# Performance work log

Measured on AMD Instinct MI355X. Metric: run time of the kernel, lower is better.

Reference implementation:

```python
import jax, jax.numpy as jnp
import numpy as np

H = 16  # heads


def setup_inputs() -> dict:
    key = jax.random.key(0)
    ks = jax.random.split(key, 10)
    B, S, M = 4, 2048, 1024
    scale = 1.0 / np.sqrt(M)
    return {
        "x": jax.random.normal(ks[0], (B, S, M), dtype=jnp.float32),
        "mask": jax.random.uniform(ks[1], (B, 1, S, S), dtype=jnp.float32),
        "Wq": jax.random.normal(ks[2], (M, M), dtype=jnp.float32) * scale,
        "bq": jax.random.normal(ks[3], (M,), dtype=jnp.float32) * scale,
        "Wk": jax.random.normal(ks[4], (M, M), dtype=jnp.float32) * scale,
        "bk": jax.random.normal(ks[5], (M,), dtype=jnp.float32) * scale,
        "Wv": jax.random.normal(ks[6], (M, M), dtype=jnp.float32) * scale,
        "bv": jax.random.normal(ks[7], (M,), dtype=jnp.float32) * scale,
        "Wo": jax.random.normal(ks[8], (M, M), dtype=jnp.float32) * scale,
        "bo": jax.random.normal(ks[9], (M,), dtype=jnp.float32) * scale,
    }


def reference(x, mask, Wq, bq, Wk, bk, Wv, bv, Wo, bo):
    B, S, M = x.shape
    dk = M // H
    # QKV projections (torch Linear: x @ W.T + b), then split heads -> [B,H,S,dk]
    q = (x @ Wq.T + bq).reshape(B, S, H, dk).transpose(0, 2, 1, 3)
    k = (x @ Wk.T + bk).reshape(B, S, H, dk).transpose(0, 2, 1, 3)
    v = (x @ Wv.T + bv).reshape(B, S, H, dk).transpose(0, 2, 1, 3)
    # scores: [B,H,S,S], multiplicative mask (non-standard!) then softmax
    scores = jnp.einsum("bhqd,bhkd->bhqk", q, k) / jnp.sqrt(jnp.float32(dk))
    scores = scores * mask  # mask broadcasts over heads
    attn = jax.nn.softmax(scores, axis=-1)
    # dropout is identity in eval/reference mode
    out = jnp.einsum("bhqk,bhkd->bhqd", attn, v)  # [B,H,S,dk]
    concat = out.transpose(0, 2, 1, 3).reshape(B, S, M)
    return concat @ Wo.T + bo
```

## Files before the change

kernel.cpp:

```cpp
#include <hip/hip_runtime.h>

typedef __attribute__((ext_vector_type(8))) short s16x8;
typedef __attribute__((ext_vector_type(4))) float f32x4;
typedef __attribute__((ext_vector_type(16))) float f32x16;
typedef __attribute__((ext_vector_type(2))) unsigned int u32x2;

#define DEV static __device__ __forceinline__

DEV void gload_lds16(const void* g, void* l) {
  __builtin_amdgcn_global_load_lds(
      (const __attribute__((address_space(1))) void*)g,
      (__attribute__((address_space(3))) void*)l, 16, 0, 0);
}

DEV unsigned short f2bf(float f) {
  unsigned int u = __float_as_uint(f);
  u = (u + 0x7fffu + ((u >> 16) & 1u)) >> 16;
  return (unsigned short)u;
}

DEV unsigned pk2(float lo, float hi) {
  unsigned r;
  asm("v_cvt_pk_bf16_f32 %0, %1, %2" : "=v"(r) : "v"(lo), "v"(hi));
  return r;
}

DEV float exp2_fast(float x) {
  float r;
  asm("v_exp_f32 %0, %1" : "=v"(r) : "v"(x));
  return r;
}

DEV void cvt8(const float* __restrict__ in, unsigned short* __restrict__ out, int i) {
  float4 a = *(const float4*)(in + i);
  float4 b = *(const float4*)(in + i + 4);
  union { s16x8 v; unsigned short u[8]; } o;
  o.u[0] = f2bf(a.x); o.u[1] = f2bf(a.y); o.u[2] = f2bf(a.z); o.u[3] = f2bf(a.w);
  o.u[4] = f2bf(b.x); o.u[5] = f2bf(b.y); o.u[6] = f2bf(b.z); o.u[7] = f2bf(b.w);
  *(s16x8*)(out + i) = o.v;
}

__global__ __launch_bounds__(256) void k_cvt(const float* __restrict__ in,
                                             unsigned short* __restrict__ out) {
  cvt8(in, out, (blockIdx.x * 256 + threadIdx.x) * 8);
}

__global__ __launch_bounds__(256) void k_cvt4(
    const float* __restrict__ a0, const float* __restrict__ a1,
    const float* __restrict__ a2, const float* __restrict__ a3,
    unsigned short* __restrict__ o0, unsigned short* __restrict__ o1,
    unsigned short* __restrict__ o2, unsigned short* __restrict__ o3) {
  const float* in; unsigned short* out;
  switch (blockIdx.y) {
    case 0: in = a0; out = o0; break;
    case 1: in = a1; out = o1; break;
    case 2: in = a2; out = o2; break;
    default: in = a3; out = o3; break;
  }
  cvt8(in, out, (blockIdx.x * 256 + threadIdx.x) * 8);
}

template <int MODE>
__global__ __launch_bounds__(256) void k_gemm(
    const unsigned short* __restrict__ A,
    const unsigned short* __restrict__ B0, const unsigned short* __restrict__ B1,
    const unsigned short* __restrict__ B2,
    const float* __restrict__ bias0, const float* __restrict__ bias1,
    const float* __restrict__ bias2,
    void* __restrict__ out0, void* __restrict__ out1, void* __restrict__ out2) {
  constexpr int K = 1024;
  __shared__ unsigned short As[128 * 64];
  __shared__ unsigned short Bs[128 * 64];

  const int z = blockIdx.z;
  const unsigned short* Bw = (z == 0) ? B0 : (z == 1) ? B1 : B2;
  const float* bias = (z == 0) ? bias0 : (z == 1) ? bias1 : bias2;
  void* outp = (z == 0) ? out0 : (z == 1) ? out1 : out2;

  const int tid = threadIdx.x;
  const int lane = tid & 63;
  const int l15 = lane & 15, g = lane >> 4;
  const int w = tid >> 6;
  const int wr = w >> 1, wc = w & 1;
  const int m0 = blockIdx.y * 128;
  const int n0 = blockIdx.x * 128;

  const int sr = tid >> 3;
  const int sc = tid & 7;

  f32x4 acc[4][4] = {};

  for (int kt = 0; kt < K / 64; ++kt) {
#pragma unroll
    for (int i = 0; i < 4; ++i) {
      const int row = i * 32 + sr;
      gload_lds16(A + (size_t)(m0 + row) * K + kt * 64 + ((sc ^ (row & 7)) * 8),
                  (void*)(As + i * 2048 + tid * 8));
      gload_lds16(Bw + (size_t)(n0 + row) * K + kt * 64 + ((sc ^ (row & 7)) * 8),
                  (void*)(Bs + i * 2048 + tid * 8));
    }
    __syncthreads();
#pragma unroll
    for (int ks = 0; ks < 2; ++ks) {
      s16x8 af[4], bf[4];
#pragma unroll
      for (int i = 0; i < 4; ++i) {
        const int ra = wr * 64 + i * 16 + l15;
        af[i] = *(const s16x8*)(As + ra * 64 + (((ks * 4 + g) ^ (ra & 7)) * 8));
        const int rb = wc * 64 + i * 16 + l15;
        bf[i] = *(const s16x8*)(Bs + rb * 64 + (((ks * 4 + g) ^ (rb & 7)) * 8));
      }
#pragma unroll
      for (int i = 0; i < 4; ++i)
#pragma unroll
        for (int j = 0; j < 4; ++j)
          acc[i][j] = __builtin_amdgcn_mfma_f32_16x16x32_bf16(af[i], bf[j], acc[i][j], 0, 0, 0);
    }
    __syncthreads();
  }

#pragma unroll
  for (int j = 0; j < 4; ++j) {
    const int gcol = n0 + wc * 64 + j * 16 + l15;
    const float bv = bias[gcol];
#pragma unroll
    for (int i = 0; i < 4; ++i) {
#pragma unroll
      for (int r = 0; r < 4; ++r) {
        const int grow = m0 + wr * 64 + i * 16 + g * 4 + r;
        const float val = acc[i][j][r] + bv;
        if (MODE == 0) {
          const int bb = grow >> 11, s = grow & 2047;
          const int h = gcol >> 6, d = gcol & 63;
          ((unsigned short*)outp)[(((size_t)(bb * 16 + h) * 2048 + s) << 6) + d] = f2bf(val);
        } else {
          ((float*)outp)[(size_t)grow * 1024 + gcol] = val;
        }
      }
    }
  }
}

__global__ __launch_bounds__(256) void k_transpose(const unsigned short* __restrict__ v,
                                                   unsigned short* __restrict__ vt) {
  __shared__ unsigned short T[64 * 72];
  const int t = threadIdx.x;
  const size_t base = (size_t)(blockIdx.z * 16 + blockIdx.y) * 2048 * 64;
  const int s0 = blockIdx.x * 64;
  {
    const int srow = t >> 2, dc = (t & 3) * 16;
    const unsigned short* src = v + base + (size_t)(s0 + srow) * 64 + dc;
    *(s16x8*)(T + srow * 72 + dc) = *(const s16x8*)src;
    *(s16x8*)(T + srow * 72 + dc + 8) = *(const s16x8*)(src + 8);
  }
  __syncthreads();
  {
    const int drow = t >> 2, scc = (t & 3) * 16;
    union { s16x8 v8; unsigned short u[8]; } o0, o1;
#pragma unroll
    for (int e = 0; e < 8; ++e) o0.u[e] = T[(scc + e) * 72 + drow];
#pragma unroll
    for (int e = 0; e < 8; ++e) o1.u[e] = T[(scc + 8 + e) * 72 + drow];
    unsigned short* dst = vt + base + (size_t)drow * 2048 + s0 + scc;
    *(s16x8*)dst = o0.v8;
    *(s16x8*)(dst + 8) = o1.v8;
  }
}

__global__ __launch_bounds__(256) void k_maskT(const float* __restrict__ mask,
                                               unsigned short* __restrict__ mT, int b0) {
  constexpr float SC = 0.125f * 1.44269504f;
  __shared__ unsigned short T[64][65];
  const int t = threadIdx.x;
  const int bz = blockIdx.z;
  const float* mb = mask + (size_t)(b0 + bz) * 2048 * 2048;
  unsigned short* ob = mT + (size_t)bz * 2048 * 2048;
  const int q0 = blockIdx.y * 64, k0 = blockIdx.x * 64;
  const int r = t >> 2, c4 = (t & 3) * 16;
  {
    const float* src = mb + (size_t)(q0 + r) * 2048 + k0 + c4;
#pragma unroll
    for (int i = 0; i < 16; i += 4) {
      float4 v = *(const float4*)(src + i);
      T[r][c4 + i + 0] = f2bf(v.x * SC);
      T[r][c4 + i + 1] = f2bf(v.y * SC);
      T[r][c4 + i + 2] = f2bf(v.z * SC);
      T[r][c4 + i + 3] = f2bf(v.w * SC);
    }
  }
  __syncthreads();
  {
    union { s16x8 v8; unsigned short u[8]; } o0, o1;
#pragma unroll
    for (int e = 0; e < 8; ++e) o0.u[e] = T[c4 + e][r];
#pragma unroll
    for (int e = 0; e < 8; ++e) o1.u[e] = T[c4 + 8 + e][r];
    unsigned short* dst = ob + (size_t)(k0 + r) * 2048 + q0 + c4;
    *(s16x8*)dst = o0.v8;
    *(s16x8*)(dst + 8) = o1.v8;
  }
}

__global__ __launch_bounds__(256) void k_attn3(
    const unsigned short* __restrict__ q, const unsigned short* __restrict__ k,
    const unsigned short* __restrict__ vt, const unsigned short* __restrict__ mT,
    unsigned short* __restrict__ concat, int b0) {
  __shared__ unsigned short Ks[2][64 * 64];
  __shared__ unsigned short Vs[2][64 * 64];
  __shared__ unsigned short Ms[2][64 * 128];

  const int tid = threadIdx.x;
  const int lane = tid & 63;
  const int w = tid >> 6;
  const int l31 = lane & 31;
  const int hh = lane >> 5;
  const int h = blockIdx.x, qt = blockIdx.y, bz = blockIdx.z;
  const int b = b0 + bz;

  const size_t bhO = (size_t)(b * 16 + h) * (2048 * 64);
  const unsigned short* kb = k + bhO;
  const unsigned short* vb = vt + bhO;
  const int q0 = qt * 128;
  const int qc = w * 32 + l31;
  const int qg = q0 + qc;

  s16x8 qf[4];
  {
    const unsigned short* qp = q + bhO + (size_t)qg * 64 + hh * 8;
#pragma unroll
    for (int kd = 0; kd < 4; ++kd) qf[kd] = *(const s16x8*)(qp + kd * 16);
  }

  const unsigned short* mtb = mT + (size_t)bz * (2048 * 2048);

  const int A2 = (qc >> 3) ^ (hh << 2);
  const unsigned short* mpp[2][4];
#pragma unroll
  for (int bu = 0; bu < 2; ++bu)
#pragma unroll
    for (int c = 0; c < 4; ++c)
      mpp[bu][c] = Ms[bu] + (qc & 7) + hh * 512 + ((A2 ^ c) * 8) + c * 128;

  float m_r = -3.0e38f, l_r = 0.f;
  f32x16 oacc[2] = {};

  const int sr = tid >> 3;
  const int sc = tid & 7;

#define STAGE(BUF, T_)                                                              \
  {                                                                                 \
    const int kv0s = (T_)*64;                                                       \
    _Pragma("unroll") for (int i = 0; i < 2; ++i) {                                 \
      const int row = i * 32 + sr;                                                  \
      const int sz = (sc ^ (row & 7)) * 8;                                          \
      gload_lds16(kb + (size_t)(kv0s + row) * 64 + sz,                              \
                  (void*)(Ks[BUF] + i * 2048 + tid * 8));                           \
      gload_lds16(vb + (size_t)row * 2048 + kv0s + sz,                              \
                  (void*)(Vs[BUF] + i * 2048 + tid * 8));                           \
    }                                                                               \
    _Pragma("unroll") for (int j = 0; j < 4; ++j) {                                 \
      const int s = j * 256 + tid;                                                  \
      const int mrow = s >> 4, mch = s & 15;                                        \
      gload_lds16(mtb + (size_t)(kv0s + mrow) * 2048 + q0 + ((mch ^ (mrow & 7)) * 8), \
                  (void*)(Ms[BUF] + j * 2048 + tid * 8));                           \
    }                                                                               \
  }

  STAGE(0, 0)
  __syncthreads();

  for (int tt = 0; tt < 16; ++tt) {
#pragma unroll
    for (int half = 0; half < 2; ++half) {
      const int t = tt * 2 + half;
      if (t < 31) STAGE(half ^ 1, t + 1)

      f32x16 sacc[2] = {};
      __builtin_amdgcn_s_setprio(1);
#pragma unroll
      for (int f = 0; f < 2; ++f) {
        const int rk = f * 32 + l31;
        const unsigned short* Kr = Ks[half] + rk * 64;
        const int swb = rk & 7;
#pragma unroll
        for (int kd = 0; kd < 4; ++kd) {
          const s16x8 kf = *(const s16x8*)(Kr + (((kd * 2 + hh) ^ swb) * 8));
          sacc[f] = __builtin_amdgcn_mfma_f32_32x32x16_bf16(kf, qf[kd], sacc[f], 0, 0, 0);
        }
      }
      __builtin_amdgcn_s_setprio(0);

      float p[32];
      float tm = -3.0e38f;
#pragma unroll
      for (int f = 0; f < 2; ++f)
#pragma unroll
        for (int r = 0; r < 16; ++r) {
          const unsigned short mu = mpp[half][r & 3][(r >> 2) * 1024 + f * 4096];
          const float mval = __uint_as_float((unsigned)mu << 16);
          const float sv = sacc[f][r] * mval;
          p[f * 16 + r] = sv;
          tm = fmaxf(tm, sv);
        }
      tm = fmaxf(tm, __shfl_xor(tm, 32, 64));
      if (__any(tm > m_r + 11.5f)) {
        const float mn = fmaxf(m_r, tm);
        const float rs = exp2_fast(m_r - mn);
        m_r = mn;
        l_r *= rs;
#pragma unroll
        for (int df = 0; df < 2; ++df)
#pragma unroll
          for (int r = 0; r < 16; ++r) oacc[df][r] *= rs;
      }
      float ps = 0.f;
#pragma unroll
      for (int n = 0; n < 32; ++n) {
        p[n] = exp2_fast(p[n] - m_r);
        ps += p[n];
      }
      ps += __shfl_xor(ps, 32, 64);
      l_r += ps;

#pragma unroll
      for (int ks = 0; ks < 4; ++ks) {
        const int pb = ks * 8;
        const unsigned X0 = pk2(p[pb + 0], p[pb + 1]);
        const unsigned X1 = pk2(p[pb + 2], p[pb + 3]);
        const unsigned Y0 = pk2(p[pb + 4], p[pb + 5]);
        const unsigned Y1 = pk2(p[pb + 6], p[pb + 7]);
        const u32x2 r0 = __builtin_amdgcn_permlane32_swap(X0, Y0, false, false);
        const u32x2 r1 = __builtin_amdgcn_permlane32_swap(X1, Y1, false, false);
        union { s16x8 v; unsigned u[4]; } pf;
        pf.u[0] = r0.x; pf.u[1] = r1.x; pf.u[2] = r0.y; pf.u[3] = r1.y;
        __builtin_amdgcn_s_setprio(1);
#pragma unroll
        for (int df = 0; df < 2; ++df) {
          const int rv = df * 32 + l31;
          const s16x8 vf =
              *(const s16x8*)(Vs[half] + rv * 64 + (((ks * 2 + hh) ^ (rv & 7)) * 8));
          oacc[df] = __builtin_amdgcn_mfma_f32_32x32x16_bf16(vf, pf.v, oacc[df], 0, 0, 0);
        }
        __builtin_amdgcn_s_setprio(0);
      }
      __syncthreads();
    }
  }
#undef STAGE

  const float inv = 1.0f / l_r;
  unsigned short* cb = concat + ((size_t)b * 2048 + qg) * 1024 + h * 64;
#pragma unroll
  for (int df = 0; df < 2; ++df)
#pragma unroll
    for (int r = 0; r < 16; r += 2) {
      const int d = df * 32 + (r & 3) + 8 * (r >> 2) + 4 * hh;
      const unsigned u = (unsigned)f2bf(oacc[df][r] * inv) |
                         ((unsigned)f2bf(oacc[df][r + 1] * inv) << 16);
      *(unsigned*)(cb + d) = u;
    }
}

extern "C" void kernel_launch(void* const* d_in, const int* in_sizes, int n_in,
                              void* d_out, int out_size, void* d_ws, size_t ws_size,
                              hipStream_t stream) {
  const float* x    = (const float*)d_in[0];
  const float* mask = (const float*)d_in[1];
  const float* Wq   = (const float*)d_in[2];
  const float* bq   = (const float*)d_in[3];
  const float* Wk   = (const float*)d_in[4];
  const float* bk   = (const float*)d_in[5];
  const float* Wv   = (const float*)d_in[6];
  const float* bv   = (const float*)d_in[7];
  const float* Wo   = (const float*)d_in[8];
  const float* bo   = (const float*)d_in[9];

  char* ws = (char*)d_ws;
  unsigned short* xb  = (unsigned short*)(ws);
  unsigned short* wqb = (unsigned short*)(ws + (size_t)16777216);
  unsigned short* wkb = (unsigned short*)(ws + (size_t)18874368);
  unsigned short* wvb = (unsigned short*)(ws + (size_t)20971520);
  unsigned short* wob = (unsigned short*)(ws + (size_t)23068672);
  unsigned short* qw  = (unsigned short*)(ws + (size_t)25165824);
  unsigned short* kw  = (unsigned short*)(ws + (size_t)41943040);
  unsigned short* vw  = (unsigned short*)(ws + (size_t)58720256);
  unsigned short* vtw = (unsigned short*)(ws + (size_t)75497472);
  unsigned short* cw  = xb;
  unsigned short* mTb = vw;

  k_cvt<<<dim3(4096), dim3(256), 0, stream>>>(x, xb);
  k_cvt4<<<dim3(512, 4), dim3(256), 0, stream>>>(Wq, Wk, Wv, Wo, wqb, wkb, wvb, wob);
  k_gemm<0><<<dim3(8, 64, 3), dim3(256), 0, stream>>>(xb, wqb, wkb, wvb, bq, bk, bv,
                                                      (void*)qw, (void*)kw, (void*)vw);
  k_transpose<<<dim3(32, 16, 4), dim3(256), 0, stream>>>(vw, vtw);
  k_maskT<<<dim3(32, 32, 2), dim3(256), 0, stream>>>(mask, mTb, 0);
  k_attn3<<<dim3(16, 16, 2), dim3(256), 0, stream>>>(qw, kw, vtw, mTb, cw, 0);
  k_maskT<<<dim3(32, 32, 2), dim3(256), 0, stream>>>(mask, mTb, 2);
  k_attn3<<<dim3(16, 16, 2), dim3(256), 0, stream>>>(qw, kw, vtw, mTb, cw, 2);
  k_gemm<1><<<dim3(8, 64, 1), dim3(256), 0, stream>>>(cw, wob, wob, wob, bo, bo, bo,
                                                      d_out, d_out, d_out);
}
```

Baseline: 275.4 us.

## Fuse QKV projections sharing A tiles; retile mask to row-major blocks

Replaces the three-way z-indexed QKV GEMM with one kernel that loads each A tile once and multiplies it against Q, K and V weight tiles, so x traffic to LDS is shared across the three projections. The mask preprocessing no longer transposes through LDS. It writes a bf16 copy laid out as one 64-key block per tile, and the attention kernel reads it with 4-wide vector LDS loads instead of scalar strided reads. This cuts the transpose and LDS work in mask prep and the LDS instruction count in the softmax loop. The cost is more accumulator registers in the QKV kernel (96 floats), which may lower occupancy.

```diff
diff --git a/kernel.cpp b/kernel.cpp
--- a/kernel.cpp
+++ b/kernel.cpp
@@ -1,6 +1,7 @@
 #include <hip/hip_runtime.h>
 
 typedef __attribute__((ext_vector_type(8))) short s16x8;
+typedef __attribute__((ext_vector_type(4))) short s16x4;
 typedef __attribute__((ext_vector_type(4))) float f32x4;
 typedef __attribute__((ext_vector_type(16))) float f32x16;
 typedef __attribute__((ext_vector_type(2))) unsigned int u32x2;
@@ -18,6 +19,8 @@
   u = (u + 0x7fffu + ((u >> 16) & 1u)) >> 16;
   return (unsigned short)u;
 }
+
+DEV float bf2f(unsigned short u) { return __uint_as_float((unsigned)u << 16); }
 
 DEV unsigned pk2(float lo, float hi) {
   unsigned r;
@@ -60,22 +63,102 @@
   cvt8(in, out, (blockIdx.x * 256 + threadIdx.x) * 8);
 }
 
-template <int MODE>
-__global__ __launch_bounds__(256) void k_gemm(
+__global__ __launch_bounds__(256) void k_gemm_qkv(
     const unsigned short* __restrict__ A,
-    const unsigned short* __restrict__ B0, const unsigned short* __restrict__ B1,
-    const unsigned short* __restrict__ B2,
-    const float* __restrict__ bias0, const float* __restrict__ bias1,
-    const float* __restrict__ bias2,
-    void* __restrict__ out0, void* __restrict__ out1, void* __restrict__ out2) {
+    const unsigned short* __restrict__ Bq, const unsigned short* __restrict__ Bk,
+    const unsigned short* __restrict__ Bv,
+    const float* __restrict__ bq, const float* __restrict__ bk,
+    const float* __restrict__ bv,
+    unsigned short* __restrict__ oq, unsigned short* __restrict__ ok,
+    unsigned short* __restrict__ ov) {
+  constexpr int K = 1024;
+  __shared__ unsigned short As[128 * 64];
+  __shared__ unsigned short Bs[3][64 * 64];
+
+  const int tid = threadIdx.x;
+  const int lane = tid & 63;
+  const int l15 = lane & 15, g = lane >> 4;
+  const int w = tid >> 6;
+  const int wr = w >> 1, wc = w & 1;
+  const int m0 = blockIdx.y * 128;
+  const int n0 = blockIdx.x * 64;
+
+  const int sr = tid >> 3;
+  const int sc = tid & 7;
+
+  const unsigned short* Bp[3] = {Bq, Bk, Bv};
+  f32x4 acc[3][4][2] = {};
+
+  for (int kt = 0; kt < K / 64; ++kt) {
+#pragma unroll
+    for (int i = 0; i < 4; ++i) {
+      const int row = i * 32 + sr;
+      gload_lds16(A + (size_t)(m0 + row) * K + kt * 64 + ((sc ^ (row & 7)) * 8),
+                  (void*)(As + i * 2048 + tid * 8));
+    }
+#pragma unroll
+    for (int z = 0; z < 3; ++z)
+#pragma unroll
+      for (int i = 0; i < 2; ++i) {
+        const int row = i * 32 + sr;
+        gload_lds16(Bp[z] + (size_t)(n0 + row) * K + kt * 64 + ((sc ^ (row & 7)) * 8),
+                    (void*)(Bs[z] + i * 2048 + tid * 8));
+      }
+    __syncthreads();
+#pragma unroll
+    for (int ks = 0; ks < 2; ++ks) {
+      s16x8 af[4];
+#pragma unroll
+      for (int mi = 0; mi < 4; ++mi) {
+        const int ra = wr * 64 + mi * 16 + l15;
+        af[mi] = *(const s16x8*)(As + ra * 64 + (((ks * 4 + g) ^ (ra & 7)) * 8));
+      }
+#pragma unroll
+      for (int z = 0; z < 3; ++z) {
+        s16x8 bf2[2];
+#pragma unroll
+        for (int nj = 0; nj < 2; ++nj) {
+          const int rb = wc * 32 + nj * 16 + l15;
+          bf2[nj] = *(const s16x8*)(Bs[z] + rb * 64 + (((ks * 4 + g) ^ (rb & 7)) * 8));
+        }
+#pragma unroll
+        for (int mi = 0; mi < 4; ++mi)
+#pragma unroll
+          for (int nj = 0; nj < 2; ++nj)
+            acc[z][mi][nj] =
+                __builtin_amdgcn_mfma_f32_16x16x32_bf16(af[mi], bf2[nj], acc[z][mi][nj], 0, 0, 0);
+      }
+    }
+    __syncthreads();
+  }
+
+  const float* biasA[3] = {bq, bk, bv};
+  unsigned short* outA[3] = {oq, ok, ov};
+#pragma unroll
+  for (int z = 0; z < 3; ++z)
+#pragma unroll
+    for (int nj = 0; nj < 2; ++nj) {
+      const int gcol = n0 + wc * 32 + nj * 16 + l15;
+      const float bvv = biasA[z][gcol];
+      const int h = gcol >> 6, d = gcol & 63;
+#pragma unroll
+      for (int mi = 0; mi < 4; ++mi)
+#pragma unroll
+        for (int r = 0; r < 4; ++r) {
+          const int grow = m0 + wr * 64 + mi * 16 + g * 4 + r;
+          const int bb = grow >> 11, s = grow & 2047;
+          outA[z][(((size_t)(bb * 16 + h) * 2048 + s) << 6) + d] =
+              f2bf(acc[z][mi][nj][r] + bvv);
+        }
+    }
+}
+
+__global__ __launch_bounds__(256) void k_gemm_o(
+    const unsigned short* __restrict__ A, const unsigned short* __restrict__ Bw,
+    const float* __restrict__ bias, float* __restrict__ outp) {
   constexpr int K = 1024;
   __shared__ unsigned short As[128 * 64];
   __shared__ unsigned short Bs[128 * 64];
-
-  const int z = blockIdx.z;
-  const unsigned short* Bw = (z == 0) ? B0 : (z == 1) ? B1 : B2;
-  const float* bias = (z == 0) ? bias0 : (z == 1) ? bias1 : bias2;
-  void* outp = (z == 0) ? out0 : (z == 1) ? out1 : out2;
 
   const int tid = threadIdx.x;
   const int lane = tid & 63;
@@ -124,20 +207,12 @@
     const int gcol = n0 + wc * 64 + j * 16 + l15;
     const float bv = bias[gcol];
 #pragma unroll
-    for (int i = 0; i < 4; ++i) {
+    for (int i = 0; i < 4; ++i)
 #pragma unroll
       for (int r = 0; r < 4; ++r) {
         const int grow = m0 + wr * 64 + i * 16 + g * 4 + r;
-        const float val = acc[i][j][r] + bv;
-        if (MODE == 0) {
-          const int bb = grow >> 11, s = grow & 2047;
-          const int h = gcol >> 6, d = gcol & 63;
-          ((unsigned short*)outp)[(((size_t)(bb * 16 + h) * 2048 + s) << 6) + d] = f2bf(val);
-        } else {
-          ((float*)outp)[(size_t)grow * 1024 + gcol] = val;
-        }
-      }
-    }
+        outp[(size_t)grow * 1024 + gcol] = acc[i][j][r] + bv;
+      }
   }
 }
 
@@ -167,47 +242,33 @@
   }
 }
 
-__global__ __launch_bounds__(256) void k_maskT(const float* __restrict__ mask,
-                                               unsigned short* __restrict__ mT, int b0) {
+__global__ __launch_bounds__(256) void k_maskR(const float* __restrict__ mask,
+                                               unsigned short* __restrict__ mR, int b0) {
   constexpr float SC = 0.125f * 1.44269504f;
-  __shared__ unsigned short T[64][65];
-  const int t = threadIdx.x;
+  const int tid = threadIdx.x;
+  const int ql = tid >> 3, c = tid & 7;
+  const int q = blockIdx.x * 32 + ql;
+  const int t = blockIdx.y;
   const int bz = blockIdx.z;
-  const float* mb = mask + (size_t)(b0 + bz) * 2048 * 2048;
-  unsigned short* ob = mT + (size_t)bz * 2048 * 2048;
-  const int q0 = blockIdx.y * 64, k0 = blockIdx.x * 64;
-  const int r = t >> 2, c4 = (t & 3) * 16;
-  {
-    const float* src = mb + (size_t)(q0 + r) * 2048 + k0 + c4;
-#pragma unroll
-    for (int i = 0; i < 16; i += 4) {
-      float4 v = *(const float4*)(src + i);
-      T[r][c4 + i + 0] = f2bf(v.x * SC);
-      T[r][c4 + i + 1] = f2bf(v.y * SC);
-      T[r][c4 + i + 2] = f2bf(v.z * SC);
-      T[r][c4 + i + 3] = f2bf(v.w * SC);
-    }
-  }
-  __syncthreads();
-  {
-    union { s16x8 v8; unsigned short u[8]; } o0, o1;
-#pragma unroll
-    for (int e = 0; e < 8; ++e) o0.u[e] = T[c4 + e][r];
-#pragma unroll
-    for (int e = 0; e < 8; ++e) o1.u[e] = T[c4 + 8 + e][r];
-    unsigned short* dst = ob + (size_t)(k0 + r) * 2048 + q0 + c4;
-    *(s16x8*)dst = o0.v8;
-    *(s16x8*)(dst + 8) = o1.v8;
-  }
+  const float* src =
+      mask + (size_t)(b0 + bz) * 4194304 + (size_t)q * 2048 + t * 64 + c * 8;
+  float4 v0 = *(const float4*)src;
+  float4 v1 = *(const float4*)(src + 4);
+  union { s16x8 v; unsigned short u[8]; } o;
+  o.u[0] = f2bf(v0.x * SC); o.u[1] = f2bf(v0.y * SC);
+  o.u[2] = f2bf(v0.z * SC); o.u[3] = f2bf(v0.w * SC);
+  o.u[4] = f2bf(v1.x * SC); o.u[5] = f2bf(v1.y * SC);
+  o.u[6] = f2bf(v1.z * SC); o.u[7] = f2bf(v1.w * SC);
+  *(s16x8*)(mR + (size_t)bz * 4194304 + (size_t)t * 131072 + (size_t)q * 64 + c * 8) = o.v;
 }
 
 __global__ __launch_bounds__(256) void k_attn3(
     const unsigned short* __restrict__ q, const unsigned short* __restrict__ k,
-    const unsigned short* __restrict__ vt, const unsigned short* __restrict__ mT,
+    const unsigned short* __restrict__ vt, const unsigned short* __restrict__ mR,
     unsigned short* __restrict__ concat, int b0) {
   __shared__ unsigned short Ks[2][64 * 64];
   __shared__ unsigned short Vs[2][64 * 64];
-  __shared__ unsigned short Ms[2][64 * 128];
+  __shared__ unsigned short Ms[2][128 * 64];
 
   const int tid = threadIdx.x;
   const int lane = tid & 63;
@@ -231,15 +292,7 @@
     for (int kd = 0; kd < 4; ++kd) qf[kd] = *(const s16x8*)(qp + kd * 16);
   }
 
-  const unsigned short* mtb = mT + (size_t)bz * (2048 * 2048);
-
-  const int A2 = (qc >> 3) ^ (hh << 2);
-  const unsigned short* mpp[2][4];
-#pragma unroll
-  for (int bu = 0; bu < 2; ++bu)
-#pragma unroll
-    for (int c = 0; c < 4; ++c)
-      mpp[bu][c] = Ms[bu] + (qc & 7) + hh * 512 + ((A2 ^ c) * 8) + c * 128;
+  const unsigned short* mtb = mR + (size_t)bz * 4194304;
 
   float m_r = -3.0e38f, l_r = 0.f;
   f32x16 oacc[2] = {};
@@ -247,23 +300,24 @@
   const int sr = tid >> 3;
   const int sc = tid & 7;
 
-#define STAGE(BUF, T_)                                                              \
-  {                                                                                 \
-    const int kv0s = (T_)*64;                                                       \
-    _Pragma("unroll") for (int i = 0; i < 2; ++i) {                                 \
-      const int row = i * 32 + sr;                                                  \
-      const int sz = (sc ^ (row & 7)) * 8;                                          \
-      gload_lds16(kb + (size_t)(kv0s + row) * 64 + sz,                              \
-                  (void*)(Ks[BUF] + i * 2048 + tid * 8));                           \
-      gload_lds16(vb + (size_t)row * 2048 + kv0s + sz,                              \
-                  (void*)(Vs[BUF] + i * 2048 + tid * 8));                           \
-    }                                                                               \
-    _Pragma("unroll") for (int j = 0; j < 4; ++j) {                                 \
-      const int s = j * 256 + tid;                                                  \
-      const int mrow = s >> 4, mch = s & 15;                                        \
-      gload_lds16(mtb + (size_t)(kv0s + mrow) * 2048 + q0 + ((mch ^ (mrow & 7)) * 8), \
-                  (void*)(Ms[BUF] + j * 2048 + tid * 8));                           \
-    }                                                                               \
+#define STAGE(BUF, T_)                                                                \
+  {                                                                                   \
+    const int kv0s = (T_)*64;                                                         \
+    _Pragma("unroll") for (int i = 0; i < 2; ++i) {                                   \
+      const int row = i * 32 + sr;                                                    \
+      const int sz = (sc ^ (row & 7)) * 8;                                            \
+      gload_lds16(kb + (size_t)(kv0s + row) * 64 + sz,                                \
+                  (void*)(Ks[BUF] + i * 2048 + tid * 8));                             \
+      gload_lds16(vb + (size_t)row * 2048 + kv0s + sz,                                \
+                  (void*)(Vs[BUF] + i * 2048 + tid * 8));                             \
+    }                                                                                 \
+    _Pragma("unroll") for (int j = 0; j < 4; ++j) {                                   \
+      const int lc = j * 256 + tid;                                                   \
+      const int qrow = lc >> 3, cl = lc & 7;                                          \
+      gload_lds16(mtb + (size_t)(T_)*131072 + (size_t)(q0 + qrow) * 64 +              \
+                      ((cl ^ (qrow & 7)) * 8),                                        \
+                  (void*)(Ms[BUF] + lc * 8));                                         \
+    }                                                                                 \
   }
 
   STAGE(0, 0)
@@ -292,16 +346,23 @@
 
       float p[32];
       float tm = -3.0e38f;
-#pragma unroll
-      for (int f = 0; f < 2; ++f)
-#pragma unroll
-        for (int r = 0; r < 16; ++r) {
-          const unsigned short mu = mpp[half][r & 3][(r >> 2) * 1024 + f * 4096];
-          const float mval = __uint_as_float((unsigned)mu << 16);
-          const float sv = sacc[f][r] * mval;
-          p[f * 16 + r] = sv;
-          tm = fmaxf(tm, sv);
-        }
+      {
+        const unsigned short* Mq = Ms[half] + qc * 64 + hh * 4;
+        const int sw = qc & 7;
+#pragma unroll
+        for (int f = 0; f < 2; ++f)
+#pragma unroll
+          for (int rq = 0; rq < 4; ++rq) {
+            const s16x4 m4 = *(const s16x4*)(Mq + (((rq + 4 * f) ^ sw) * 8));
+#pragma unroll
+            for (int j = 0; j < 4; ++j) {
+              const int r = 4 * rq + j;
+              const float sv = sacc[f][r] * bf2f((unsigned short)m4[j]);
+              p[f * 16 + r] = sv;
+              tm = fmaxf(tm, sv);
+            }
+          }
+      }
       tm = fmaxf(tm, __shfl_xor(tm, 32, 64));
       if (__any(tm > m_r + 11.5f)) {
         const float mn = fmaxf(m_r, tm);
@@ -386,17 +447,16 @@
   unsigned short* vw  = (unsigned short*)(ws + (size_t)58720256);
   unsigned short* vtw = (unsigned short*)(ws + (size_t)75497472);
   unsigned short* cw  = xb;
-  unsigned short* mTb = vw;
+  unsigned short* mRb = vw;
 
   k_cvt<<<dim3(4096), dim3(256), 0, stream>>>(x, xb);
   k_cvt4<<<dim3(512, 4), dim3(256), 0, stream>>>(Wq, Wk, Wv, Wo, wqb, wkb, wvb, wob);
-  k_gemm<0><<<dim3(8, 64, 3), dim3(256), 0, stream>>>(xb, wqb, wkb, wvb, bq, bk, bv,
-                                                      (void*)qw, (void*)kw, (void*)vw);
+  k_gemm_qkv<<<dim3(16, 64), dim3(256), 0, stream>>>(xb, wqb, wkb, wvb, bq, bk, bv,
+                                                     qw, kw, vw);
   k_transpose<<<dim3(32, 16, 4), dim3(256), 0, stream>>>(vw, vtw);
-  k_maskT<<<dim3(32, 32, 2), dim3(256), 0, stream>>>(mask, mTb, 0);
-  k_attn3<<<dim3(16, 16, 2), dim3(256), 0, stream>>>(qw, kw, vtw, mTb, cw, 0);
-  k_maskT<<<dim3(32, 32, 2), dim3(256), 0, stream>>>(mask, mTb, 2);
-  k_attn3<<<dim3(16, 16, 2), dim3(256), 0, stream>>>(qw, kw, vtw, mTb, cw, 2);
-  k_gemm<1><<<dim3(8, 64, 1), dim3(256), 0, stream>>>(cw, wob, wob, wob, bo, bo, bo,
-                                                      d_out, d_out, d_out);
-}
+  k_maskR<<<dim3(64, 32, 2), dim3(256), 0, stream>>>(mask, mRb, 0);
+  k_attn3<<<dim3(16, 16, 2), dim3(256), 0, stream>>>(qw, kw, vtw, mRb, cw, 0);
+  k_maskR<<<dim3(64, 32, 2), dim3(256), 0, stream>>>(mask, mRb, 2);
+  k_attn3<<<dim3(16, 16, 2), dim3(256), 0, stream>>>(qw, kw, vtw, mRb, cw, 2);
+  k_gemm_o<<<dim3(8, 64), dim3(256), 0, stream>>>(cw, wob, bo, (float*)d_out);
+}
```

New measurement: 305.5 us. +10.9%, slower.
